# Optimization experiments

Hardware: AMD Instinct MI355X
Metric: run time of the kernel (lower is better)

Reference implementation:

```python
import jax, jax.numpy as jnp
import numpy as np

BN_EPS = 1e-5

def _bn_relu(x, gamma, beta, mean, var):
    # x: [B, N, C]; BatchNorm1d(N) in eval mode normalizes over dim=1 (N)
    inv = jax.lax.rsqrt(var + BN_EPS)
    scale = (gamma * inv)[None, :, None]
    shift = (beta - mean * gamma * inv)[None, :, None]
    return jax.nn.relu(x * scale + shift)

def _forward(x, q_gamma, q_beta, q_mean, q_var,
             k_gamma, k_beta, k_mean, k_var,
             v_gamma, v_beta, v_mean, v_var,
             Wq, Wk, Wv, Wp):
    B, C, H, W = x.shape
    N = H * W
    E = Wq.shape[0]
    xs = x.reshape(B, C, N).transpose(0, 2, 1)  # [B, N, C]
    # BN+ReLU over spatial axis, then Linear(N->E) on spatial axis per channel -> [B, E, C]
    q = jnp.einsum('bnc,en->bec', _bn_relu(xs, q_gamma, q_beta, q_mean, q_var), Wq)
    k = jnp.einsum('bnc,en->bec', _bn_relu(xs, k_gamma, k_beta, k_mean, k_var), Wk)
    v = jnp.einsum('bnc,en->bec', _bn_relu(xs, v_gamma, v_beta, v_mean, v_var), Wv)
    scores = jnp.einsum('bec,bfc->bef', q, k) / jnp.sqrt(jnp.asarray(E, x.dtype))  # [B, E, E]
    attn = jax.nn.softmax(scores, axis=-1)
    out = jnp.einsum('bef,bfc->bec', attn, v)          # [B, E, C]
    out = jnp.einsum('bec,ne->bcn', out, Wp)            # Linear(E->N) -> [B, C, N]
    return out.reshape(B, C, H, W)

def setup_inputs() -> dict:
    key = jax.random.key(0)
    ks = jax.random.split(key, 20)
    B, C, H, W = 32, 512, 32, 32
    N = H * W  # sp_dim = 1024
    E = 1024   # embed_dim
    d = {'x': jax.random.normal(ks[0], (B, C, H, W), jnp.float32)}
    i = 1
    for p in ('q', 'k', 'v'):
        d[f'{p}_gamma'] = jax.random.uniform(ks[i], (N,), jnp.float32, 0.5, 1.5); i += 1
        d[f'{p}_beta'] = 0.1 * jax.random.normal(ks[i], (N,), jnp.float32); i += 1
        d[f'{p}_mean'] = 0.1 * jax.random.normal(ks[i], (N,), jnp.float32); i += 1
        d[f'{p}_var'] = jax.random.uniform(ks[i], (N,), jnp.float32, 0.5, 1.5); i += 1
    # torch Linear weight layout: [out, in]; scale ~ 1/sqrt(fan_in)
    d['Wq'] = jax.random.normal(ks[i], (E, N), jnp.float32) * (1.0 / np.sqrt(N)); i += 1
    d['Wk'] = jax.random.normal(ks[i], (E, N), jnp.float32) * (1.0 / np.sqrt(N)); i += 1
    d['Wv'] = jax.random.normal(ks[i], (E, N), jnp.float32) * (1.0 / np.sqrt(N)); i += 1
    d['Wp'] = jax.random.normal(ks[i], (N, E), jnp.float32) * (1.0 / np.sqrt(E)); i += 1
    return d

def reference(x, q_gamma, q_beta, q_mean, q_var,
              k_gamma, k_beta, k_mean, k_var,
              v_gamma, v_beta, v_mean, v_var,
              Wq, Wk, Wv, Wp):
    return _forward(x, q_gamma, q_beta, q_mean, q_var,
                    k_gamma, k_beta, k_mean, k_var,
                    v_gamma, v_beta, v_mean, v_var,
                    Wq, Wk, Wv, Wp)
```

## Files before the change

kernel.cpp:

```cpp
#include <hip/hip_runtime.h>
#include <math.h>

#define BN_EPS 1e-5f

namespace {

constexpr int Bb = 32;
constexpr int Cc = 512;
constexpr int Nn = 1024;
constexpr int Ee = 1024;

typedef __attribute__((ext_vector_type(8))) short short8;
typedef __attribute__((ext_vector_type(4))) float f32x4;
typedef __attribute__((ext_vector_type(4))) unsigned short ushort4_t;

struct bfpair { unsigned short h, l; };

__device__ __forceinline__ unsigned short bf16_rne(float v) {
  unsigned u = __builtin_bit_cast(unsigned, v);
  unsigned r = u + 0x7FFFu + ((u >> 16) & 1u);
  return (unsigned short)(r >> 16);
}
__device__ __forceinline__ float bf16_to_f(unsigned short h) {
  unsigned u = ((unsigned)h) << 16;
  return __builtin_bit_cast(float, u);
}
__device__ __forceinline__ bfpair split_bf(float v) {
  bfpair p;
  p.h = bf16_rne(v);
  p.l = bf16_rne(v - bf16_to_f(p.h));
  return p;
}

__device__ __forceinline__ void gll16(const void* g, void* l) {
  __builtin_amdgcn_global_load_lds(
      (const __attribute__((address_space(1))) void*)g,
      (__attribute__((address_space(3))) void*)l, 16, 0, 0);
}

__global__ __launch_bounds__(256) void prep3(
    const float* __restrict__ qg, const float* __restrict__ qb,
    const float* __restrict__ qm, const float* __restrict__ qv,
    const float* __restrict__ kg, const float* __restrict__ kb,
    const float* __restrict__ km, const float* __restrict__ kv,
    const float* __restrict__ vg, const float* __restrict__ vb,
    const float* __restrict__ vm, const float* __restrict__ vv,
    float* __restrict__ hdr) {
  int i = blockIdx.x * blockDim.x + threadIdx.x;
  if (i < 1024) {
    float inv, sc;
    inv = rsqrtf(qv[i] + BN_EPS); sc = qg[i] * inv;
    hdr[i] = sc;          hdr[1024 + i] = qb[i] - qm[i] * sc;
    inv = rsqrtf(kv[i] + BN_EPS); sc = kg[i] * inv;
    hdr[2048 + i] = sc;   hdr[3072 + i] = kb[i] - km[i] * sc;
    inv = rsqrtf(vv[i] + BN_EPS); sc = vg[i] * inv;
    hdr[4096 + i] = sc;   hdr[5120 + i] = vb[i] - vm[i] * sc;
  }
}

__global__ __launch_bounds__(256) void convert_w(
    const float* __restrict__ wsrc, unsigned short* __restrict__ wh,
    unsigned short* __restrict__ wl, long total4) {
  for (long i = (long)blockIdx.x * 256 + threadIdx.x; i < total4; i += (long)gridDim.x * 256) {
    float4 v = ((const float4*)wsrc)[i];
    bfpair p0 = split_bf(v.x), p1 = split_bf(v.y), p2 = split_bf(v.z), p3 = split_bf(v.w);
    ushort4_t hv, lv;
    hv.x = p0.h; hv.y = p1.h; hv.z = p2.h; hv.w = p3.h;
    lv.x = p0.l; lv.y = p1.l; lv.z = p2.l; lv.w = p3.l;
    *(ushort4_t*)&wh[i * 4] = hv;
    *(ushort4_t*)&wl[i * 4] = lv;
  }
}

__global__ __launch_bounds__(256) void convert_y3(
    const float* __restrict__ x, const float* __restrict__ hdr,
    unsigned short* __restrict__ yqh, unsigned short* __restrict__ yql,
    unsigned short* __restrict__ ykh, unsigned short* __restrict__ ykl,
    unsigned short* __restrict__ dout_us, long b0, long total4) {
  const float* sq = hdr;        const float* tq = hdr + 1024;
  const float* sk = hdr + 2048; const float* tk = hdr + 3072;
  const float* sv = hdr + 4096; const float* tv = hdr + 5120;
  for (long i = (long)blockIdx.x * 256 + threadIdx.x; i < total4; i += (long)gridDim.x * 256) {
    float4 v = ((const float4*)x)[i];
    int n4 = (int)(i & 255);
    float4 a, b;
    ushort4_t hv, lv;
    a = ((const float4*)sq)[n4]; b = ((const float4*)tq)[n4];
    {
      bfpair p0 = split_bf(fmaxf(fmaf(v.x, a.x, b.x), 0.f));
      bfpair p1 = split_bf(fmaxf(fmaf(v.y, a.y, b.y), 0.f));
      bfpair p2 = split_bf(fmaxf(fmaf(v.z, a.z, b.z), 0.f));
      bfpair p3 = split_bf(fmaxf(fmaf(v.w, a.w, b.w), 0.f));
      hv.x = p0.h; hv.y = p1.h; hv.z = p2.h; hv.w = p3.h;
      lv.x = p0.l; lv.y = p1.l; lv.z = p2.l; lv.w = p3.l;
      *(ushort4_t*)&yqh[i * 4] = hv; *(ushort4_t*)&yql[i * 4] = lv;
    }
    a = ((const float4*)sk)[n4]; b = ((const float4*)tk)[n4];
    {
      bfpair p0 = split_bf(fmaxf(fmaf(v.x, a.x, b.x), 0.f));
      bfpair p1 = split_bf(fmaxf(fmaf(v.y, a.y, b.y), 0.f));
      bfpair p2 = split_bf(fmaxf(fmaf(v.z, a.z, b.z), 0.f));
      bfpair p3 = split_bf(fmaxf(fmaf(v.w, a.w, b.w), 0.f));
      hv.x = p0.h; hv.y = p1.h; hv.z = p2.h; hv.w = p3.h;
      lv.x = p0.l; lv.y = p1.l; lv.z = p2.l; lv.w = p3.l;
      *(ushort4_t*)&ykh[i * 4] = hv; *(ushort4_t*)&ykl[i * 4] = lv;
    }
    a = ((const float4*)sv)[n4]; b = ((const float4*)tv)[n4];
    {
      bfpair p0 = split_bf(fmaxf(fmaf(v.x, a.x, b.x), 0.f));
      bfpair p1 = split_bf(fmaxf(fmaf(v.y, a.y, b.y), 0.f));
      bfpair p2 = split_bf(fmaxf(fmaf(v.z, a.z, b.z), 0.f));
      bfpair p3 = split_bf(fmaxf(fmaf(v.w, a.w, b.w), 0.f));
      hv.x = p0.h; hv.y = p1.h; hv.z = p2.h; hv.w = p3.h;
      lv.x = p0.l; lv.y = p1.l; lv.z = p2.l; lv.w = p3.l;
      long g = i >> 17;
      long local = i & 131071;
      unsigned short* slot = dout_us + (b0 + g) * 1048576L;
      *(ushort4_t*)&slot[local * 4] = hv;
      *(ushort4_t*)&slot[524288 + local * 4] = lv;
    }
  }
}

#define MFMA16 __builtin_amdgcn_mfma_f32_16x16x32_bf16

template<bool SPLIT, bool MFIRST, int BM, int BMODE>
__global__ __launch_bounds__(512, 2) void gemm3p(
    const unsigned short* __restrict__ Ah, const unsigned short* __restrict__ Al,
    long ldA, long bsA,
    const unsigned short* __restrict__ Bh0, const unsigned short* __restrict__ Bl0,
    const unsigned short* __restrict__ Bh1, const unsigned short* __restrict__ Bl1,
    int msel, long ldB, long bsB,
    float* __restrict__ Cf, unsigned short* __restrict__ Chi, unsigned short* __restrict__ Clo,
    long ldC, long bsC, int K, float alpha, int g0, int g1) {
  constexpr int WH = BM / 2;
  constexpr int AF = WH / 16;
  constexpr int NB = (BMODE == 0) ? 2 : 1;
  __shared__ unsigned short sA[2][2][BM][32];
  __shared__ unsigned short sB[2][NB][256][32];

  const int nb = gridDim.x;
  int f = blockIdx.x;
  if ((nb & 7) == 0) f = (f & 7) * (nb >> 3) + (f >> 3);
  const int i0 = f % g0, i1 = (f / g0) % g1;
  const long zb = f / (g0 * g1);
  const int m0 = (MFIRST ? i0 : i1) * BM;
  const int n0 = (MFIRST ? i1 : i0) * 256;

  const int t = threadIdx.x, lane = t & 63, w = t >> 6;
  const int wr = w >> 2, wc = w & 3;
  const int sr  = lane >> 2;
  const int skc = (((lane & 3) ^ ((lane >> 3) & 3)) * 8);
  const int fr = lane & 15;
  const int kq = ((((lane >> 4) & 3) ^ ((fr >> 1) & 3)) * 8);

  const unsigned short* Bh = (m0 >= msel) ? Bh1 : Bh0;
  const unsigned short* Bl = (m0 >= msel) ? Bl1 : Bl0;
  if (BMODE == 1) Bl = Bh;

  const int aw = w & 3, ahl = w >> 2;
  const unsigned short* a0;
  const unsigned short* a1 = nullptr;
  if (BM == 256) {
    a0 = Ah + zb * bsA + (long)(m0 + w * 32 + sr) * ldA + skc;
    a1 = Al + zb * bsA + (long)(m0 + w * 32 + sr) * ldA + skc;
  } else {
    a0 = (ahl ? Al : Ah) + zb * bsA + (long)(m0 + aw * 32 + sr) * ldA + skc;
  }
  const unsigned short* b0 = Bh + zb * bsB + (long)(n0 + w * 32 + sr) * ldB + skc;
  const unsigned short* b1 = Bl + zb * bsB + (long)(n0 + w * 32 + sr) * ldB + skc;
  const long a16 = 16 * ldA, b16 = 16 * ldB;

  auto STAGE = [&](int buf) {
    if constexpr (BM == 256) {
      gll16(a0, &sA[buf][0][w * 32][0]);  gll16(a0 + a16, &sA[buf][0][w * 32 + 16][0]);
      gll16(a1, &sA[buf][1][w * 32][0]);  gll16(a1 + a16, &sA[buf][1][w * 32 + 16][0]);
      a0 += 32; a1 += 32;
    } else {
      gll16(a0, &sA[buf][ahl][aw * 32][0]);
      gll16(a0 + a16, &sA[buf][ahl][aw * 32 + 16][0]);
      a0 += 32;
    }
    gll16(b0, &sB[buf][0][w * 32][0]);  gll16(b0 + b16, &sB[buf][0][w * 32 + 16][0]);
    b0 += 32;
    if constexpr (BMODE == 0) {
      gll16(b1, &sB[buf][NB - 1][w * 32][0]);
      gll16(b1 + b16, &sB[buf][NB - 1][w * 32 + 16][0]);
      b1 += 32;
    }
  };

  f32x4 acc[AF][4] = {};
  const int nt = K >> 5;

  STAGE(0);
  STAGE(1);
  int cur = 0;

  for (int it = 0; it < nt; ++it) {
    if (it + 1 < nt) {
      if constexpr (BM == 256)      asm volatile("s_waitcnt vmcnt(8)" ::: "memory");
      else if constexpr (BMODE == 0) asm volatile("s_waitcnt vmcnt(6)" ::: "memory");
      else                           asm volatile("s_waitcnt vmcnt(4)" ::: "memory");
    } else {
      asm volatile("s_waitcnt vmcnt(0)" ::: "memory");
    }
    asm volatile("s_barrier" ::: "memory");

    short8 bh[4], bl[4], ah[4], al[4];
#pragma unroll
    for (int j = 0; j < 4; ++j) {
      bh[j] = *(const short8*)&sB[cur][0][wc * 64 + j * 16 + fr][kq];
      if (BMODE == 0)
        bl[j] = *(const short8*)&sB[cur][NB - 1][wc * 64 + j * 16 + fr][kq];
    }
#pragma unroll
    for (int i = 0; i < 4; ++i) {
      ah[i] = *(const short8*)&sA[cur][0][wr * WH + i * 16 + fr][kq];
      al[i] = *(const short8*)&sA[cur][1][wr * WH + i * 16 + fr][kq];
    }

    if constexpr (BM == 256) {
      __builtin_amdgcn_s_setprio(1);
#pragma unroll
      for (int i = 0; i < 4; ++i)
#pragma unroll
        for (int j = 0; j < 4; ++j) {
          acc[i][j] = MFMA16(ah[i], bh[j], acc[i][j], 0, 0, 0);
          if (BMODE == 0) acc[i][j] = MFMA16(ah[i], bl[j], acc[i][j], 0, 0, 0);
          acc[i][j] = MFMA16(al[i], bh[j], acc[i][j], 0, 0, 0);
        }
      __builtin_amdgcn_s_setprio(0);
#pragma unroll
      for (int i = 0; i < 4; ++i) {
        ah[i] = *(const short8*)&sA[cur][0][wr * WH + (i + 4) * 16 + fr][kq];
        al[i] = *(const short8*)&sA[cur][1][wr * WH + (i + 4) * 16 + fr][kq];
      }
      asm volatile("s_waitcnt lgkmcnt(0)" ::: "memory");
      asm volatile("s_barrier" ::: "memory");
      if (it + 2 < nt) STAGE(cur);
      __builtin_amdgcn_s_setprio(1);
#pragma unroll
      for (int i = 0; i < 4; ++i)
#pragma unroll
        for (int j = 0; j < 4; ++j) {
          acc[i + 4][j] = MFMA16(ah[i], bh[j], acc[i + 4][j], 0, 0, 0);
          if (BMODE == 0) acc[i + 4][j] = MFMA16(ah[i], bl[j], acc[i + 4][j], 0, 0, 0);
          acc[i + 4][j] = MFMA16(al[i], bh[j], acc[i + 4][j], 0, 0, 0);
        }
      __builtin_amdgcn_s_setprio(0);
    } else {
      asm volatile("s_waitcnt lgkmcnt(0)" ::: "memory");
      asm volatile("s_barrier" ::: "memory");
      if (it + 2 < nt) STAGE(cur);
      __builtin_amdgcn_s_setprio(1);
#pragma unroll
      for (int i = 0; i < 4; ++i)
#pragma unroll
        for (int j = 0; j < 4; ++j) {
          acc[i][j] = MFMA16(ah[i], bh[j], acc[i][j], 0, 0, 0);
          if (BMODE == 0) acc[i][j] = MFMA16(ah[i], bl[j], acc[i][j], 0, 0, 0);
          acc[i][j] = MFMA16(al[i], bh[j], acc[i][j], 0, 0, 0);
        }
      __builtin_amdgcn_s_setprio(0);
    }
    cur ^= 1;
  }

  const int rb = ((lane >> 4) & 3) * 4;
#pragma unroll
  for (int i = 0; i < AF; ++i)
#pragma unroll
    for (int j = 0; j < 4; ++j) {
      long col = n0 + wc * 64 + j * 16 + fr;
#pragma unroll
      for (int v = 0; v < 4; ++v) {
        long row = m0 + wr * WH + i * 16 + rb + v;
        float val = acc[i][j][v] * alpha;
        long idx = zb * bsC + row * ldC + col;
        if (SPLIT) {
          bfpair p = split_bf(val);
          Chi[idx] = p.h;
          Clo[idx] = p.l;
        } else {
          Cf[idx] = val;
        }
      }
    }
}

__global__ __launch_bounds__(256) void softmax_rows(float* __restrict__ S) {
  long row = blockIdx.x;
  float* p = S + row * 1024;
  int t = threadIdx.x;
  float4 v = *(float4*)(p + 4 * t);
  float mx = fmaxf(fmaxf(v.x, v.y), fmaxf(v.z, v.w));
#pragma unroll
  for (int i = 1; i < 64; i <<= 1) mx = fmaxf(mx, __shfl_xor(mx, i));
  __shared__ float redm[4];
  __shared__ float reds[4];
  int wave = t >> 6, lane = t & 63;
  if (lane == 0) redm[wave] = mx;
  __syncthreads();
  mx = fmaxf(fmaxf(redm[0], redm[1]), fmaxf(redm[2], redm[3]));
  float e0 = expf(v.x - mx), e1 = expf(v.y - mx);
  float e2 = expf(v.z - mx), e3 = expf(v.w - mx);
  float sum = (e0 + e1) + (e2 + e3);
#pragma unroll
  for (int i = 1; i < 64; i <<= 1) sum += __shfl_xor(sum, i);
  if (lane == 0) reds[wave] = sum;
  __syncthreads();
  sum = (reds[0] + reds[1]) + (reds[2] + reds[3]);
  float inv = 1.0f / sum;
  ushort4_t hv;
  hv.x = bf16_rne(e0 * inv);
  hv.y = bf16_rne(e1 * inv);
  hv.z = bf16_rne(e2 * inv);
  hv.w = bf16_rne(e3 * inv);
  unsigned short* ph = (unsigned short*)p;
  *(ushort4_t*)&ph[4 * t] = hv;
}

}

extern "C" void kernel_launch(void* const* d_in, const int* in_sizes, int n_in,
                              void* d_out, int out_size, void* d_ws, size_t ws_size,
                              hipStream_t stream) {
  const float* x  = (const float*)d_in[0];
  const float* qg = (const float*)d_in[1];
  const float* qb = (const float*)d_in[2];
  const float* qm = (const float*)d_in[3];
  const float* qv = (const float*)d_in[4];
  const float* kg = (const float*)d_in[5];
  const float* kb = (const float*)d_in[6];
  const float* km = (const float*)d_in[7];
  const float* kv = (const float*)d_in[8];
  const float* vg = (const float*)d_in[9];
  const float* vb = (const float*)d_in[10];
  const float* vm = (const float*)d_in[11];
  const float* vv = (const float*)d_in[12];
  const float* Wq = (const float*)d_in[13];
  const float* Wk = (const float*)d_in[14];
  const float* Wv = (const float*)d_in[15];
  const float* Wp = (const float*)d_in[16];

  const size_t wFix = 65536 + 16UL * 1024 * 1024;
  const size_t perB = 12UL * 1024 * 1024;
  int G = 32;
  while (G > 1 && wFix + (size_t)G * perB > ws_size) G >>= 1;

  char* ws = (char*)d_ws;
  float* hdr = (float*)ws;

  const long WE = 1024L * 1024;
  unsigned short* WQKh = (unsigned short*)(ws + 65536);
  unsigned short* WQKl = WQKh + 2 * WE;
  unsigned short* Wvh  = WQKl + 2 * WE;
  unsigned short* Wvl  = Wvh + WE;
  unsigned short* Wph  = Wvl + WE;
  unsigned short* Wpl  = Wph + WE;

  const long YB = 524288;
  unsigned short* yqh = Wpl + WE;
  unsigned short* yql = yqh + (long)G * YB;
  unsigned short* ykh = yql + (long)G * YB;
  unsigned short* ykl = ykh + (long)G * YB;
  const long QKBS = 1048576;
  unsigned short* QKh = ykl + (long)G * YB;
  unsigned short* QKl = QKh + (long)G * QKBS;
  float* S = (float*)(QKl + (long)G * QKBS);

  unsigned short* dout_us = (unsigned short*)d_out;

  dim3 blk(256);
  const int BIG = 1 << 30;

  prep3<<<dim3(4), blk, 0, stream>>>(qg, qb, qm, qv, kg, kb, km, kv, vg, vb, vm, vv, hdr);

  const long W4 = WE / 4;
  convert_w<<<dim3(1024), blk, 0, stream>>>(Wq, WQKh, WQKl, W4);
  convert_w<<<dim3(1024), blk, 0, stream>>>(Wk, WQKh + WE, WQKl + WE, W4);
  convert_w<<<dim3(1024), blk, 0, stream>>>(Wv, Wvh, Wvl, W4);
  convert_w<<<dim3(1024), blk, 0, stream>>>(Wp, Wph, Wpl, W4);

  for (int b0 = 0; b0 < Bb; b0 += G) {
    const float* xg = x + (size_t)b0 * Cc * Nn;

    convert_y3<<<dim3(2048), blk, 0, stream>>>(
        xg, hdr, yqh, yql, ykh, ykl, dout_us, b0, (long)G * 131072);

    gemm3p<true, true, 256, 0><<<dim3(8 * 2 * G), dim3(512), 0, stream>>>(
        WQKh, WQKl, Nn, 0L,
        yqh, yql, ykh, ykl, 1024, Nn, YB,
        nullptr, QKh, QKl, Cc, QKBS, Nn, 1.0f, 8, 2);

    gemm3p<false, false, 256, 0><<<dim3(4 * 4 * G), dim3(512), 0, stream>>>(
        QKh, QKl, Cc, QKBS,
        QKh + 524288, QKl + 524288, nullptr, nullptr, BIG, Cc, QKBS,
        S, nullptr, nullptr, Ee, 1048576L, Cc, 0.03125f, 4, 4);

    softmax_rows<<<dim3(G * Ee), blk, 0, stream>>>(S);

    gemm3p<true, false, 128, 0><<<dim3(4 * 4 * G), dim3(512), 0, stream>>>(
        dout_us + (long)b0 * 1048576, dout_us + (long)b0 * 1048576 + 524288, Nn, 1048576L,
        Wvh, Wvl, nullptr, nullptr, BIG, Nn, 0L,
        nullptr, yqh, yql, Ee, YB, Nn, 1.0f, 4, 4);

    gemm3p<true, false, 128, 1><<<dim3(4 * 4 * G), dim3(512), 0, stream>>>(
        yqh, yql, Ee, YB,
        (unsigned short*)S, nullptr, nullptr, nullptr, BIG,
        2L * Ee, 2097152L,
        nullptr, QKh, QKl, Ee, QKBS, Ee, 1.0f, 4, 4);

    gemm3p<false, false, 128, 0><<<dim3(4 * 4 * G), dim3(512), 0, stream>>>(
        QKh, QKl, Ee, QKBS,
        Wph, Wpl, nullptr, nullptr, BIG, Ee, 0L,
        (float*)d_out + (size_t)b0 * Cc * Nn, nullptr, nullptr,
        Nn, (long)Cc * Nn, Ee, 1.0f, 4, 4);
  }
}
```

Measured before the change: 702.0 us.

## Switch GEMM to triple-buffered LDS pipeline and drop 256-row tile variant

The GEMM kernel now uses three LDS stages and issues the next-next stage load right after the top-of-loop barrier. This removes the second barrier and lgkmcnt wait inside each K iteration. The BM=256 variant is removed, so the QK projection and score GEMMs use 128-row tiles with twice as many blocks. LDS use grows to three buffers, which may limit occupancy, and the smaller tiles reload more operand data.

```diff
diff --git a/kernel.cpp b/kernel.cpp
--- a/kernel.cpp
+++ b/kernel.cpp
@@ -124,7 +124,7 @@
 
 #define MFMA16 __builtin_amdgcn_mfma_f32_16x16x32_bf16
 
-template<bool SPLIT, bool MFIRST, int BM, int BMODE>
+template<bool SPLIT, bool MFIRST, int BMODE>
 __global__ __launch_bounds__(512, 2) void gemm3p(
     const unsigned short* __restrict__ Ah, const unsigned short* __restrict__ Al,
     long ldA, long bsA,
@@ -133,18 +133,17 @@
     int msel, long ldB, long bsB,
     float* __restrict__ Cf, unsigned short* __restrict__ Chi, unsigned short* __restrict__ Clo,
     long ldC, long bsC, int K, float alpha, int g0, int g1) {
-  constexpr int WH = BM / 2;
-  constexpr int AF = WH / 16;
+  constexpr int WH = 64;
   constexpr int NB = (BMODE == 0) ? 2 : 1;
-  __shared__ unsigned short sA[2][2][BM][32];
-  __shared__ unsigned short sB[2][NB][256][32];
+  __shared__ unsigned short sA[3][2][128][32];
+  __shared__ unsigned short sB[3][NB][256][32];
 
   const int nb = gridDim.x;
   int f = blockIdx.x;
   if ((nb & 7) == 0) f = (f & 7) * (nb >> 3) + (f >> 3);
   const int i0 = f % g0, i1 = (f / g0) % g1;
   const long zb = f / (g0 * g1);
-  const int m0 = (MFIRST ? i0 : i1) * BM;
+  const int m0 = (MFIRST ? i0 : i1) * 128;
   const int n0 = (MFIRST ? i1 : i0) * 256;
 
   const int t = threadIdx.x, lane = t & 63, w = t >> 6;
@@ -159,28 +158,16 @@
   if (BMODE == 1) Bl = Bh;
 
   const int aw = w & 3, ahl = w >> 2;
-  const unsigned short* a0;
-  const unsigned short* a1 = nullptr;
-  if (BM == 256) {
-    a0 = Ah + zb * bsA + (long)(m0 + w * 32 + sr) * ldA + skc;
-    a1 = Al + zb * bsA + (long)(m0 + w * 32 + sr) * ldA + skc;
-  } else {
-    a0 = (ahl ? Al : Ah) + zb * bsA + (long)(m0 + aw * 32 + sr) * ldA + skc;
-  }
+  const unsigned short* a0 =
+      (ahl ? Al : Ah) + zb * bsA + (long)(m0 + aw * 32 + sr) * ldA + skc;
   const unsigned short* b0 = Bh + zb * bsB + (long)(n0 + w * 32 + sr) * ldB + skc;
   const unsigned short* b1 = Bl + zb * bsB + (long)(n0 + w * 32 + sr) * ldB + skc;
   const long a16 = 16 * ldA, b16 = 16 * ldB;
 
   auto STAGE = [&](int buf) {
-    if constexpr (BM == 256) {
-      gll16(a0, &sA[buf][0][w * 32][0]);  gll16(a0 + a16, &sA[buf][0][w * 32 + 16][0]);
-      gll16(a1, &sA[buf][1][w * 32][0]);  gll16(a1 + a16, &sA[buf][1][w * 32 + 16][0]);
-      a0 += 32; a1 += 32;
-    } else {
-      gll16(a0, &sA[buf][ahl][aw * 32][0]);
-      gll16(a0 + a16, &sA[buf][ahl][aw * 32 + 16][0]);
-      a0 += 32;
-    }
+    gll16(a0, &sA[buf][ahl][aw * 32][0]);
+    gll16(a0 + a16, &sA[buf][ahl][aw * 32 + 16][0]);
+    a0 += 32;
     gll16(b0, &sB[buf][0][w * 32][0]);  gll16(b0 + b16, &sB[buf][0][w * 32 + 16][0]);
     b0 += 32;
     if constexpr (BMODE == 0) {
@@ -190,22 +177,22 @@
     }
   };
 
-  f32x4 acc[AF][4] = {};
+  f32x4 acc[4][4] = {};
   const int nt = K >> 5;
 
   STAGE(0);
   STAGE(1);
-  int cur = 0;
 
   for (int it = 0; it < nt; ++it) {
+    const int cur = it % 3;
     if (it + 1 < nt) {
-      if constexpr (BM == 256)      asm volatile("s_waitcnt vmcnt(8)" ::: "memory");
-      else if constexpr (BMODE == 0) asm volatile("s_waitcnt vmcnt(6)" ::: "memory");
-      else                           asm volatile("s_waitcnt vmcnt(4)" ::: "memory");
+      if constexpr (BMODE == 0) asm volatile("s_waitcnt vmcnt(6)" ::: "memory");
+      else                      asm volatile("s_waitcnt vmcnt(4)" ::: "memory");
     } else {
       asm volatile("s_waitcnt vmcnt(0)" ::: "memory");
     }
     asm volatile("s_barrier" ::: "memory");
+    if (it + 2 < nt) STAGE((it + 2) % 3);
 
     short8 bh[4], bl[4], ah[4], al[4];
 #pragma unroll
@@ -219,57 +206,21 @@
       ah[i] = *(const short8*)&sA[cur][0][wr * WH + i * 16 + fr][kq];
       al[i] = *(const short8*)&sA[cur][1][wr * WH + i * 16 + fr][kq];
     }
-
-    if constexpr (BM == 256) {
-      __builtin_amdgcn_s_setprio(1);
-#pragma unroll
-      for (int i = 0; i < 4; ++i)
-#pragma unroll
-        for (int j = 0; j < 4; ++j) {
-          acc[i][j] = MFMA16(ah[i], bh[j], acc[i][j], 0, 0, 0);
-          if (BMODE == 0) acc[i][j] = MFMA16(ah[i], bl[j], acc[i][j], 0, 0, 0);
-          acc[i][j] = MFMA16(al[i], bh[j], acc[i][j], 0, 0, 0);
-        }
-      __builtin_amdgcn_s_setprio(0);
-#pragma unroll
-      for (int i = 0; i < 4; ++i) {
-        ah[i] = *(const short8*)&sA[cur][0][wr * WH + (i + 4) * 16 + fr][kq];
-        al[i] = *(const short8*)&sA[cur][1][wr * WH + (i + 4) * 16 + fr][kq];
+    __builtin_amdgcn_s_setprio(1);
+#pragma unroll
+    for (int i = 0; i < 4; ++i)
+#pragma unroll
+      for (int j = 0; j < 4; ++j) {
+        acc[i][j] = MFMA16(ah[i], bh[j], acc[i][j], 0, 0, 0);
+        if (BMODE == 0) acc[i][j] = MFMA16(ah[i], bl[j], acc[i][j], 0, 0, 0);
+        acc[i][j] = MFMA16(al[i], bh[j], acc[i][j], 0, 0, 0);
       }
-      asm volatile("s_waitcnt lgkmcnt(0)" ::: "memory");
-      asm volatile("s_barrier" ::: "memory");
-      if (it + 2 < nt) STAGE(cur);
-      __builtin_amdgcn_s_setprio(1);
-#pragma unroll
-      for (int i = 0; i < 4; ++i)
-#pragma unroll
-        for (int j = 0; j < 4; ++j) {
-          acc[i + 4][j] = MFMA16(ah[i], bh[j], acc[i + 4][j], 0, 0, 0);
-          if (BMODE == 0) acc[i + 4][j] = MFMA16(ah[i], bl[j], acc[i + 4][j], 0, 0, 0);
-          acc[i + 4][j] = MFMA16(al[i], bh[j], acc[i + 4][j], 0, 0, 0);
-        }
-      __builtin_amdgcn_s_setprio(0);
-    } else {
-      asm volatile("s_waitcnt lgkmcnt(0)" ::: "memory");
-      asm volatile("s_barrier" ::: "memory");
-      if (it + 2 < nt) STAGE(cur);
-      __builtin_amdgcn_s_setprio(1);
-#pragma unroll
-      for (int i = 0; i < 4; ++i)
-#pragma unroll
-        for (int j = 0; j < 4; ++j) {
-          acc[i][j] = MFMA16(ah[i], bh[j], acc[i][j], 0, 0, 0);
-          if (BMODE == 0) acc[i][j] = MFMA16(ah[i], bl[j], acc[i][j], 0, 0, 0);
-          acc[i][j] = MFMA16(al[i], bh[j], acc[i][j], 0, 0, 0);
-        }
-      __builtin_amdgcn_s_setprio(0);
-    }
-    cur ^= 1;
+    __builtin_amdgcn_s_setprio(0);
   }
 
   const int rb = ((lane >> 4) & 3) * 4;
 #pragma unroll
-  for (int i = 0; i < AF; ++i)
+  for (int i = 0; i < 4; ++i)
 #pragma unroll
     for (int j = 0; j < 4; ++j) {
       long col = n0 + wc * 64 + j * 16 + fr;
@@ -389,30 +340,30 @@
     convert_y3<<<dim3(2048), blk, 0, stream>>>(
         xg, hdr, yqh, yql, ykh, ykl, dout_us, b0, (long)G * 131072);
 
-    gemm3p<true, true, 256, 0><<<dim3(8 * 2 * G), dim3(512), 0, stream>>>(
+    gemm3p<true, true, 0><<<dim3(16 * 2 * G), dim3(512), 0, stream>>>(
         WQKh, WQKl, Nn, 0L,
         yqh, yql, ykh, ykl, 1024, Nn, YB,
-        nullptr, QKh, QKl, Cc, QKBS, Nn, 1.0f, 8, 2);
-
-    gemm3p<false, false, 256, 0><<<dim3(4 * 4 * G), dim3(512), 0, stream>>>(
+        nullptr, QKh, QKl, Cc, QKBS, Nn, 1.0f, 16, 2);
+
+    gemm3p<false, false, 0><<<dim3(4 * 8 * G), dim3(512), 0, stream>>>(
         QKh, QKl, Cc, QKBS,
         QKh + 524288, QKl + 524288, nullptr, nullptr, BIG, Cc, QKBS,
-        S, nullptr, nullptr, Ee, 1048576L, Cc, 0.03125f, 4, 4);
+        S, nullptr, nullptr, Ee, 1048576L, Cc, 0.03125f, 4, 8);
 
     softmax_rows<<<dim3(G * Ee), blk, 0, stream>>>(S);
 
-    gemm3p<true, false, 128, 0><<<dim3(4 * 4 * G), dim3(512), 0, stream>>>(
+    gemm3p<true, false, 0><<<dim3(4 * 4 * G), dim3(512), 0, stream>>>(
         dout_us + (long)b0 * 1048576, dout_us + (long)b0 * 1048576 + 524288, Nn, 1048576L,
         Wvh, Wvl, nullptr, nullptr, BIG, Nn, 0L,
         nullptr, yqh, yql, Ee, YB, Nn, 1.0f, 4, 4);
 
-    gemm3p<true, false, 128, 1><<<dim3(4 * 4 * G), dim3(512), 0, stream>>>(
+    gemm3p<true, false, 1><<<dim3(4 * 4 * G), dim3(512), 0, stream>>>(
         yqh, yql, Ee, YB,
         (unsigned short*)S, nullptr, nullptr, nullptr, BIG,
         2L * Ee, 2097152L,
         nullptr, QKh, QKl, Ee, QKBS, Ee, 1.0f, 4, 4);
 
-    gemm3p<false, false, 128, 0><<<dim3(4 * 4 * G), dim3(512), 0, stream>>>(
+    gemm3p<false, false, 0><<<dim3(4 * 4 * G), dim3(512), 0, stream>>>(
         QKh, QKl, Ee, QKBS,
         Wph, Wpl, nullptr, nullptr, BIG, Ee, 0L,
         (float*)d_out + (size_t)b0 * Cc * Nn, nullptr, nullptr,
```

Result: slower. 802.0 us (+14.2%).
